# Optimization experiments

Hardware: AMD Instinct MI355X
Metric: run time of the kernel (lower is better)

## Reference

```python
import jax, jax.numpy as jnp
import numpy as np
import math

INPUT_SIZE = 20
HIDDEN = 1500
OUTPUT = 20
MLP_HID = math.ceil(5 / 4 * HIDDEN)  # 1875
T = 4096


def setup_inputs() -> dict:
    key = jax.random.key(0)
    ks = jax.random.split(key, 10)
    s_lstm = 1.0 / np.sqrt(HIDDEN)
    s1 = 1.0 / np.sqrt(HIDDEN)
    s2 = 1.0 / np.sqrt(MLP_HID)
    return {
        "input_seq": jax.random.normal(ks[0], (T, INPUT_SIZE), dtype=jnp.float32),
        "W_ih": jax.random.uniform(ks[1], (4 * HIDDEN, INPUT_SIZE), jnp.float32, -s_lstm, s_lstm),
        "W_hh": jax.random.uniform(ks[2], (4 * HIDDEN, HIDDEN), jnp.float32, -s_lstm, s_lstm),
        "b_ih": jax.random.uniform(ks[3], (4 * HIDDEN,), jnp.float32, -s_lstm, s_lstm),
        "b_hh": jax.random.uniform(ks[4], (4 * HIDDEN,), jnp.float32, -s_lstm, s_lstm),
        "W1": jax.random.uniform(ks[5], (MLP_HID, HIDDEN), jnp.float32, -s1, s1),
        "b1": jax.random.uniform(ks[6], (MLP_HID,), jnp.float32, -s1, s1),
        "W2": jax.random.uniform(ks[7], (OUTPUT, MLP_HID), jnp.float32, -s2, s2),
        "b2": jax.random.uniform(ks[8], (OUTPUT,), jnp.float32, -s2, s2),
    }


def reference(input_seq, W_ih, W_hh, b_ih, b_hh, W1, b1, W2, b2):
    H = W_hh.shape[1]
    # Precompute input contribution for all timesteps: (T, 4H)
    x_proj = input_seq @ W_ih.T + (b_ih + b_hh)

    def step(carry, xp):
        h, c = carry
        gates = xp + h @ W_hh.T  # (4H,)
        i, f, g, o = jnp.split(gates, 4)
        i = jax.nn.sigmoid(i)
        f = jax.nn.sigmoid(f)
        g = jnp.tanh(g)
        o = jax.nn.sigmoid(o)
        c_new = f * c + i * g
        h_new = o * jnp.tanh(c_new)
        return (h_new, c_new), None

    h0 = jnp.zeros((H,), dtype=input_seq.dtype)
    c0 = jnp.zeros((H,), dtype=input_seq.dtype)
    (h_last, _), _ = jax.lax.scan(step, (h0, c0), x_proj)
    # Dropout is identity in eval mode. Module returns predictions[-1],
    # which only depends on the last hidden state.
    hid = h_last @ W1.T + b1
    return hid @ W2.T + b2
```

## Files before the change

kernel.cpp:

```cpp
#include <hip/hip_runtime.h>
#include <math.h>

#define TT 4096
#define HH 1500
#define NB 250
#define NT 512
#define NREP 8

typedef unsigned uv4 __attribute__((ext_vector_type(4)));
typedef _Float16 h2f __attribute__((ext_vector_type(2)));
typedef _Float16 h4f __attribute__((ext_vector_type(4)));

#define ALD4(p)   __hip_atomic_load((p), __ATOMIC_RELAXED, __HIP_MEMORY_SCOPE_AGENT)
#define AST4(p,v) __hip_atomic_store((p), (v), __ATOMIC_RELAXED, __HIP_MEMORY_SCOPE_AGENT)

__device__ __forceinline__ float fast_sigmoid(float z) {
  return 1.0f / (1.0f + __expf(-z));
}
__device__ __forceinline__ float fast_tanh(float z) {
  float az = fabsf(z);
  float e  = __expf(-2.0f * az);
  float r  = (1.0f - e) / (1.0f + e);
  return copysignf(r, z);
}
__device__ __forceinline__ float dot2(unsigned wb, unsigned hb, float acc) {
#if __has_builtin(__builtin_amdgcn_fdot2)
  return __builtin_amdgcn_fdot2(__builtin_bit_cast(h2f, wb),
                                __builtin_bit_cast(h2f, hb), acc, false);
#else
  h2f w = __builtin_bit_cast(h2f, wb), h = __builtin_bit_cast(h2f, hb);
  acc = fmaf((float)w.x, (float)h.x, acc);
  return fmaf((float)w.y, (float)h.y, acc);
#endif
}

__device__ __forceinline__ uv4 pollld(const unsigned* a) {
  uv4 v;
  asm volatile("global_load_dwordx4 %0, %1, off sc0 sc1\n\t"
               "s_waitcnt vmcnt(0)"
               : "=&v"(v) : "v"(a) : "memory");
  return v;
}
__device__ __forceinline__ h4f cvt4h(uv4 v) {
  h4f r;
  r.x = (_Float16)__uint_as_float(v.x);
  r.y = (_Float16)__uint_as_float(v.y);
  r.z = (_Float16)__uint_as_float(v.z);
  r.w = (_Float16)__uint_as_float(v.w);
  return r;
}

__global__
__attribute__((amdgpu_flat_work_group_size(NT, NT), amdgpu_waves_per_eu(2, 2)))
void lstm_fused(
    const float* __restrict__ x,
    const float* __restrict__ Wih,
    const float* __restrict__ Whh,
    const float* __restrict__ bih,
    const float* __restrict__ bhh,
    const float* __restrict__ W1,
    const float* __restrict__ b1,
    const float* __restrict__ W2,
    const float* __restrict__ b2,
    float* __restrict__ out,
    unsigned* __restrict__ ws)
{
  const int tid = threadIdx.x;
  const int bid = blockIdx.x;
  const int wv  = tid >> 6;
  const int ln  = tid & 63;

  unsigned* pub  = ws;
  unsigned* hidp = ws + NREP * 2 * 1536;

  __shared__ __align__(16) _Float16 lds_wh[24 * 1536];
  __shared__ __align__(16) _Float16 lds_hh[1536];
  __shared__ __align__(16) float    lds_hf[1536];
  __shared__ float lds_xp[2][24];
  __shared__ float lds_gs[4][6];
  float* lds_hd = (float*)lds_wh;

  for (int hi = tid; hi < 24 * 1536; hi += NT) {
    const int r = hi / 1536, k = hi - r * 1536;
    const int u = r >> 2, g = r & 3;
    const size_t grow = (size_t)(g * HH + bid * 6 + u) * HH;
    const float v = (k < HH) ? Whh[grow + k] : 0.f;
    lds_wh[hi] = (_Float16)v;
  }
  if (tid < 36) lds_hh[1500 + tid] = (_Float16)0.f;

  const int uu = (wv < 6) ? wv : 0;
  const uv4* wp = ((const uv4*)lds_wh) + (size_t)uu * 4 * 192;
  const uv4* hp = (const uv4*)lds_hh;

  float4 wx0, wx1, wx2, wx3, wx4;
  float4 xr0, xr1, xr2, xr3, xr4;
  float bias = 0.f;
  if (wv == 6 && ln < 24) {
    const int g = ln / 6, u = ln - g * 6;
    const int row = g * HH + bid * 6 + u;
    const float4* s = (const float4*)(Wih + row * 20);
    wx0 = s[0]; wx1 = s[1]; wx2 = s[2]; wx3 = s[3]; wx4 = s[4];
    bias = bih[row] + bhh[row];
    const float4* xx = (const float4*)x;
    xr0 = xx[0]; xr1 = xx[1]; xr2 = xx[2]; xr3 = xx[3]; xr4 = xx[4];
  }

  float c = 0.f;

  if (tid < 6 * NREP)
    AST4(pub + (tid / 6) * 3072 + 6 * bid + (tid % 6), 1u);

  __syncthreads();

  unsigned* myrep = pub + (bid & (NREP - 1)) * 3072;

  for (int t = 0; t < TT; ++t) {
    const int s = t & 1;
    const unsigned tag = (unsigned)((t + 1) & 15);

    uv4 pw[12];
    if (wv < 6) {
      #pragma unroll
      for (int g = 0; g < 4; ++g) {
        #pragma unroll
        for (int m = 0; m < 3; ++m) pw[g * 3 + m] = wp[g * 192 + ln + 64 * m];
      }
      const int ck = (wv << 6) | ln;
      if (ck < 375) {
        unsigned* ap = myrep + s * 1536 + (ck << 2);
        uv4 v;
        for (;;) {
          v = pollld(ap);
          const unsigned miss = ((v.x & 15u) ^ tag) | ((v.y & 15u) ^ tag)
                              | ((v.z & 15u) ^ tag) | ((v.w & 15u) ^ tag);
          if (!miss) break;
          __builtin_amdgcn_s_sleep(1);
        }
        *(h4f*)(lds_hh + (ck << 2)) = cvt4h(v);
      }
    } else if (wv == 6 && ln < 24) {
      float sx = bias;
      sx += wx0.x*xr0.x + wx0.y*xr0.y + wx0.z*xr0.z + wx0.w*xr0.w;
      sx += wx1.x*xr1.x + wx1.y*xr1.y + wx1.z*xr1.z + wx1.w*xr1.w;
      sx += wx2.x*xr2.x + wx2.y*xr2.y + wx2.z*xr2.z + wx2.w*xr2.w;
      sx += wx3.x*xr3.x + wx3.y*xr3.y + wx3.z*xr3.z + wx3.w*xr3.w;
      sx += wx4.x*xr4.x + wx4.y*xr4.y + wx4.z*xr4.z + wx4.w*xr4.w;
      lds_xp[s][ln] = sx;
    }
    __syncthreads();

    if (wv < 6) {
      uv4 hv[3];
      #pragma unroll
      for (int m = 0; m < 3; ++m) hv[m] = hp[ln + 64 * m];
      float a[4] = {0.f, 0.f, 0.f, 0.f};
      #pragma unroll
      for (int g = 0; g < 4; ++g) {
        #pragma unroll
        for (int m = 0; m < 3; ++m) {
          const uv4 q = pw[g * 3 + m], h = hv[m];
          a[g] = dot2(q.x, h.x, a[g]);
          a[g] = dot2(q.y, h.y, a[g]);
          a[g] = dot2(q.z, h.z, a[g]);
          a[g] = dot2(q.w, h.w, a[g]);
        }
      }
      #pragma unroll
      for (int g = 0; g < 4; ++g) {
        a[g] += __shfl_xor(a[g], 16, 64);
        a[g] += __shfl_xor(a[g], 32, 64);
      }
      const int q4 = ln >> 4;
      float v = (q4 == 0) ? a[0] : (q4 == 1) ? a[1] : (q4 == 2) ? a[2] : a[3];
      v += __shfl_xor(v, 1, 64);
      v += __shfl_xor(v, 2, 64);
      v += __shfl_xor(v, 4, 64);
      v += __shfl_xor(v, 8, 64);
      if ((ln & 15) == 0) lds_gs[q4][wv] = v;
    } else if (wv == 6 && ln < 24 && (t + 1) < TT) {
      const float4* xx = (const float4*)(x + 20 * (t + 1));
      xr0 = xx[0]; xr1 = xx[1]; xr2 = xx[2]; xr3 = xx[3]; xr4 = xx[4];
    }
    __syncthreads();

    if (wv == 7) {
      unsigned bits = 0u;
      if (ln < 6) {
        const int u = ln;
        const float zi = lds_gs[0][u] + lds_xp[s][0 + u];
        const float zf = lds_gs[1][u] + lds_xp[s][6 + u];
        const float zg = lds_gs[2][u] + lds_xp[s][12 + u];
        const float zo = lds_gs[3][u] + lds_xp[s][18 + u];
        const float ig = fast_sigmoid(zi);
        const float fg = fast_sigmoid(zf);
        const float gg = fast_tanh(zg);
        const float og = fast_sigmoid(zo);
        c = fg * c + ig * gg;
        const float hn = og * fast_tanh(c);
        bits = (__float_as_uint(hn) & ~15u) | (unsigned)((t + 2) & 15);
      }
      const int u6 = ln % 6;
      const unsigned myb = (unsigned)__shfl((int)bits, u6, 64);
      if (ln < 6 * NREP) {
        const int rep = ln / 6;
        AST4(pub + rep * 3072 + ((t + 1) & 1) * 1536 + 6 * bid + u6, myb);
      }
    }
  }

  {
    const unsigned tagf = (unsigned)((TT + 1) & 15);
    if (tid < 375) {
      unsigned* ap = myrep + (tid << 2);
      uv4 v;
      for (;;) {
        v = pollld(ap);
        const unsigned miss = ((v.x & 15u) ^ tagf) | ((v.y & 15u) ^ tagf)
                            | ((v.z & 15u) ^ tagf) | ((v.w & 15u) ^ tagf);
        if (!miss) break;
        __builtin_amdgcn_s_sleep(1);
      }
      float4 f = {__uint_as_float(v.x), __uint_as_float(v.y),
                  __uint_as_float(v.z), __uint_as_float(v.w)};
      *(float4*)(lds_hf + (tid << 2)) = f;
    } else if (tid < 384) {
      float4 z4 = {0.f, 0.f, 0.f, 0.f};
      *(float4*)(lds_hf + (tid << 2)) = z4;
    }
  }
  __syncthreads();

  {
    const float4* h4 = (const float4*)lds_hf;
    const int r = bid + 250 * wv;
    if (r < 1875) {
      const float4* wrow = (const float4*)(W1 + (size_t)r * HH);
      float ss = 0.f;
      #pragma unroll
      for (int m = 0; m < 6; ++m) {
        const int idx = ln + 64 * m;
        if (idx < 375) {
          const float4 a = wrow[idx], hv = h4[idx];
          ss += a.x*hv.x + a.y*hv.y + a.z*hv.z + a.w*hv.w;
        }
      }
      #pragma unroll
      for (int off = 32; off > 0; off >>= 1) ss += __shfl_xor(ss, off, 64);
      if (ln == 0) {
        const float vv = ss + b1[r];
        AST4(hidp + r, (__float_as_uint(vv) & ~15u) | 5u);
      }
    }
  }
  if (bid != 0) return;

  __syncthreads();
  for (int j = tid; j < 1875; j += NT) {
    unsigned bts;
    for (;;) {
      bts = ALD4(hidp + j);
      if ((bts & 15u) == 5u) break;
      __builtin_amdgcn_s_sleep(1);
    }
    lds_hd[j] = __uint_as_float(bts);
  }
  __syncthreads();

  for (int r = wv; r < 20; r += 8) {
    float ss = 0.f;
    for (int k = ln; k < 1875; k += 64)
      ss = fmaf(W2[(size_t)r * 1875 + k], lds_hd[k], ss);
    #pragma unroll
    for (int off = 32; off > 0; off >>= 1) ss += __shfl_xor(ss, off, 64);
    if (ln == 0) out[r] = ss + b2[r];
  }
}

extern "C" void kernel_launch(void* const* d_in, const int* in_sizes, int n_in,
                              void* d_out, int out_size, void* d_ws, size_t ws_size,
                              hipStream_t stream) {
  const float* x   = (const float*)d_in[0];
  const float* Wih = (const float*)d_in[1];
  const float* Whh = (const float*)d_in[2];
  const float* bih = (const float*)d_in[3];
  const float* bhh = (const float*)d_in[4];
  const float* W1  = (const float*)d_in[5];
  const float* b1  = (const float*)d_in[6];
  const float* W2  = (const float*)d_in[7];
  const float* b2  = (const float*)d_in[8];
  float* out   = (float*)d_out;
  unsigned* ws = (unsigned*)d_ws;

  hipLaunchKernelGGL(lstm_fused, dim3(NB), dim3(NT), 0, stream,
                     x, Wih, Whh, bih, bhh, W1, b1, W2, b2, out, ws);
}
```

Measured before the change: 10.75 ms.

## Pad each block's published hidden slice to its own 64-byte line

The global exchange buffer is re-laid out so each block's six hidden values sit in their own 16-word (64-byte) line instead of being packed contiguously, six per block. The publishing wave now writes that line with 64-bit atomic stores, and each poller reads one line with two 16-byte loads. The aim is to stop several blocks writing into the same cache line, which causes false sharing and extra coherence traffic on the per-step polling path. The cost is a larger buffer, more bytes read per poll, and unaligned 32-bit LDS writes when repacking to fp16. The final readout of the hidden state also drops the zero padding of lds_hf above index 1500, which the later MLP reads may or may not rely on.

```diff
diff --git a/kernel.cpp b/kernel.cpp
--- a/kernel.cpp
+++ b/kernel.cpp
@@ -6,13 +6,15 @@
 #define NB 250
 #define NT 512
 #define NREP 8
+#define LINE 16
+#define SLOT (NB * LINE)
 
 typedef unsigned uv4 __attribute__((ext_vector_type(4)));
 typedef _Float16 h2f __attribute__((ext_vector_type(2)));
-typedef _Float16 h4f __attribute__((ext_vector_type(4)));
 
 #define ALD4(p)   __hip_atomic_load((p), __ATOMIC_RELAXED, __HIP_MEMORY_SCOPE_AGENT)
 #define AST4(p,v) __hip_atomic_store((p), (v), __ATOMIC_RELAXED, __HIP_MEMORY_SCOPE_AGENT)
+#define AST8(p,v) __hip_atomic_store((p), (v), __ATOMIC_RELAXED, __HIP_MEMORY_SCOPE_AGENT)
 
 __device__ __forceinline__ float fast_sigmoid(float z) {
   return 1.0f / (1.0f + __expf(-z));
@@ -34,20 +36,18 @@
 #endif
 }
 
-__device__ __forceinline__ uv4 pollld(const unsigned* a) {
-  uv4 v;
-  asm volatile("global_load_dwordx4 %0, %1, off sc0 sc1\n\t"
+__device__ __forceinline__ void poll2(const unsigned* a0, const unsigned* a1,
+                                      uv4& v0, uv4& v1) {
+  asm volatile("global_load_dwordx4 %0, %2, off sc0 sc1\n\t"
+               "global_load_dwordx4 %1, %3, off sc0 sc1\n\t"
                "s_waitcnt vmcnt(0)"
-               : "=&v"(v) : "v"(a) : "memory");
-  return v;
-}
-__device__ __forceinline__ h4f cvt4h(uv4 v) {
-  h4f r;
-  r.x = (_Float16)__uint_as_float(v.x);
-  r.y = (_Float16)__uint_as_float(v.y);
-  r.z = (_Float16)__uint_as_float(v.z);
-  r.w = (_Float16)__uint_as_float(v.w);
-  return r;
+               : "=&v"(v0), "=&v"(v1) : "v"(a0), "v"(a1) : "memory");
+}
+__device__ __forceinline__ unsigned packh(unsigned a, unsigned b) {
+  h2f p;
+  p.x = (_Float16)__uint_as_float(a);
+  p.y = (_Float16)__uint_as_float(b);
+  return __builtin_bit_cast(unsigned, p);
 }
 
 __global__
@@ -71,7 +71,7 @@
   const int ln  = tid & 63;
 
   unsigned* pub  = ws;
-  unsigned* hidp = ws + NREP * 2 * 1536;
+  unsigned* hidp = ws + NREP * 2 * SLOT;
 
   __shared__ __align__(16) _Float16 lds_wh[24 * 1536];
   __shared__ __align__(16) _Float16 lds_hh[1536];
@@ -108,12 +108,14 @@
 
   float c = 0.f;
 
-  if (tid < 6 * NREP)
-    AST4(pub + (tid / 6) * 3072 + 6 * bid + (tid % 6), 1u);
+  if (tid < 16 * NREP) {
+    const int rep = tid >> 4, k = tid & 15;
+    AST4(pub + rep * (2 * SLOT) + bid * LINE + k, 1u);
+  }
 
   __syncthreads();
 
-  unsigned* myrep = pub + (bid & (NREP - 1)) * 3072;
+  unsigned* myrep = pub + (bid & (NREP - 1)) * (2 * SLOT);
 
   for (int t = 0; t < TT; ++t) {
     const int s = t & 1;
@@ -127,17 +129,21 @@
         for (int m = 0; m < 3; ++m) pw[g * 3 + m] = wp[g * 192 + ln + 64 * m];
       }
       const int ck = (wv << 6) | ln;
-      if (ck < 375) {
-        unsigned* ap = myrep + s * 1536 + (ck << 2);
-        uv4 v;
+      if (ck < NB) {
+        unsigned* ap = myrep + s * SLOT + (ck << 4);
+        uv4 v0, v1;
         for (;;) {
-          v = pollld(ap);
-          const unsigned miss = ((v.x & 15u) ^ tag) | ((v.y & 15u) ^ tag)
-                              | ((v.z & 15u) ^ tag) | ((v.w & 15u) ^ tag);
+          poll2(ap, ap + 4, v0, v1);
+          const unsigned miss = ((v0.x & 15u) ^ tag) | ((v0.y & 15u) ^ tag)
+                              | ((v0.z & 15u) ^ tag) | ((v0.w & 15u) ^ tag)
+                              | ((v1.x & 15u) ^ tag) | ((v1.y & 15u) ^ tag);
           if (!miss) break;
           __builtin_amdgcn_s_sleep(1);
         }
-        *(h4f*)(lds_hh + (ck << 2)) = cvt4h(v);
+        unsigned* hd = (unsigned*)lds_hh;
+        hd[3 * ck]     = packh(v0.x, v0.y);
+        hd[3 * ck + 1] = packh(v0.z, v0.w);
+        hd[3 * ck + 2] = packh(v1.x, v1.y);
       }
     } else if (wv == 6 && ln < 24) {
       float sx = bias;
@@ -200,33 +206,37 @@
         const float hn = og * fast_tanh(c);
         bits = (__float_as_uint(hn) & ~15u) | (unsigned)((t + 2) & 15);
       }
-      const int u6 = ln % 6;
-      const unsigned myb = (unsigned)__shfl((int)bits, u6, 64);
-      if (ln < 6 * NREP) {
-        const int rep = ln / 6;
-        AST4(pub + rep * 3072 + ((t + 1) & 1) * 1536 + 6 * bid + u6, myb);
-      }
+      const unsigned tag2 = (unsigned)((t + 2) & 15);
+      const int rep = ln >> 3, k2 = (ln & 7) << 1;
+      const unsigned s0 = (unsigned)__shfl((int)bits, k2 & 7, 64);
+      const unsigned s1 = (unsigned)__shfl((int)bits, (k2 + 1) & 7, 64);
+      const unsigned d0 = (k2 < 6) ? s0 : tag2;
+      const unsigned d1 = (k2 + 1 < 6) ? s1 : tag2;
+      const unsigned long long dd =
+          (unsigned long long)d0 | ((unsigned long long)d1 << 32);
+      AST8((unsigned long long*)(pub + rep * (2 * SLOT) +
+                                 ((t + 1) & 1) * SLOT + bid * LINE + k2), dd);
     }
   }
 
   {
     const unsigned tagf = (unsigned)((TT + 1) & 15);
-    if (tid < 375) {
-      unsigned* ap = myrep + (tid << 2);
-      uv4 v;
+    if (tid < NB) {
+      unsigned* ap = myrep + (tid << 4);
+      uv4 v0, v1;
       for (;;) {
-        v = pollld(ap);
-        const unsigned miss = ((v.x & 15u) ^ tagf) | ((v.y & 15u) ^ tagf)
-                            | ((v.z & 15u) ^ tagf) | ((v.w & 15u) ^ tagf);
+        poll2(ap, ap + 4, v0, v1);
+        const unsigned miss = ((v0.x & 15u) ^ tagf) | ((v0.y & 15u) ^ tagf)
+                            | ((v0.z & 15u) ^ tagf) | ((v0.w & 15u) ^ tagf)
+                            | ((v1.x & 15u) ^ tagf) | ((v1.y & 15u) ^ tagf);
         if (!miss) break;
         __builtin_amdgcn_s_sleep(1);
       }
-      float4 f = {__uint_as_float(v.x), __uint_as_float(v.y),
-                  __uint_as_float(v.z), __uint_as_float(v.w)};
-      *(float4*)(lds_hf + (tid << 2)) = f;
-    } else if (tid < 384) {
-      float4 z4 = {0.f, 0.f, 0.f, 0.f};
-      *(float4*)(lds_hf + (tid << 2)) = z4;
+      float2* fo = (float2*)(lds_hf + 6 * tid);
+      float2 f0 = {__uint_as_float(v0.x), __uint_as_float(v0.y)};
+      float2 f1 = {__uint_as_float(v0.z), __uint_as_float(v0.w)};
+      float2 f2 = {__uint_as_float(v1.x), __uint_as_float(v1.y)};
+      fo[0] = f0; fo[1] = f1; fo[2] = f2;
     }
   }
   __syncthreads();
```

Result: slower. 11.75 ms (+9.3%).

## Dedicate one wave to h polling, double-buffer h in LDS, fuse gate activation

Applied to the files above, without the earlier changes.

Wave 7 now polls the whole published hidden-state vector with six batched loads per lane and a wave-wide any-check, instead of six compute waves each polling one chunk. The h vector in LDS is double-buffered, and each compute wave applies the gate activations and the cell update itself and publishes its own unit. This removes one __syncthreads per timestep and the lds_gs round trip on the serial critical path. In exchange all polling traffic sits on a single wave and the shuffles per compute wave increase.

```diff
diff --git a/kernel.cpp b/kernel.cpp
--- a/kernel.cpp
+++ b/kernel.cpp
@@ -34,12 +34,26 @@
 #endif
 }
 
-__device__ __forceinline__ uv4 pollld(const unsigned* a) {
-  uv4 v;
-  asm volatile("global_load_dwordx4 %0, %1, off sc0 sc1\n\t"
+__device__ __forceinline__ void poll6(const unsigned* a0, const unsigned* a1,
+                                      const unsigned* a2, const unsigned* a3,
+                                      const unsigned* a4, const unsigned* a5,
+                                      uv4& v0, uv4& v1, uv4& v2,
+                                      uv4& v3, uv4& v4, uv4& v5) {
+  asm volatile("global_load_dwordx4 %0, %6, off sc0 sc1\n\t"
+               "global_load_dwordx4 %1, %7, off sc0 sc1\n\t"
+               "global_load_dwordx4 %2, %8, off sc0 sc1\n\t"
+               "global_load_dwordx4 %3, %9, off sc0 sc1\n\t"
+               "global_load_dwordx4 %4, %10, off sc0 sc1\n\t"
+               "global_load_dwordx4 %5, %11, off sc0 sc1\n\t"
                "s_waitcnt vmcnt(0)"
-               : "=&v"(v) : "v"(a) : "memory");
-  return v;
+               : "=&v"(v0), "=&v"(v1), "=&v"(v2),
+                 "=&v"(v3), "=&v"(v4), "=&v"(v5)
+               : "v"(a0), "v"(a1), "v"(a2), "v"(a3), "v"(a4), "v"(a5)
+               : "memory");
+}
+__device__ __forceinline__ unsigned chk4(uv4 v, unsigned tag) {
+  return ((v.x & 15u) ^ tag) | ((v.y & 15u) ^ tag)
+       | ((v.z & 15u) ^ tag) | ((v.w & 15u) ^ tag);
 }
 __device__ __forceinline__ h4f cvt4h(uv4 v) {
   h4f r;
@@ -74,10 +88,9 @@
   unsigned* hidp = ws + NREP * 2 * 1536;
 
   __shared__ __align__(16) _Float16 lds_wh[24 * 1536];
-  __shared__ __align__(16) _Float16 lds_hh[1536];
+  __shared__ __align__(16) _Float16 lds_hh[2][1536];
   __shared__ __align__(16) float    lds_hf[1536];
   __shared__ float lds_xp[2][24];
-  __shared__ float lds_gs[4][6];
   float* lds_hd = (float*)lds_wh;
 
   for (int hi = tid; hi < 24 * 1536; hi += NT) {
@@ -87,11 +100,10 @@
     const float v = (k < HH) ? Whh[grow + k] : 0.f;
     lds_wh[hi] = (_Float16)v;
   }
-  if (tid < 36) lds_hh[1500 + tid] = (_Float16)0.f;
+  if (tid < 72) lds_hh[tid / 36][1500 + (tid % 36)] = (_Float16)0.f;
 
   const int uu = (wv < 6) ? wv : 0;
   const uv4* wp = ((const uv4*)lds_wh) + (size_t)uu * 4 * 192;
-  const uv4* hp = (const uv4*)lds_hh;
 
   float4 wx0, wx1, wx2, wx3, wx4;
   float4 xr0, xr1, xr2, xr3, xr4;
@@ -99,8 +111,8 @@
   if (wv == 6 && ln < 24) {
     const int g = ln / 6, u = ln - g * 6;
     const int row = g * HH + bid * 6 + u;
-    const float4* s = (const float4*)(Wih + row * 20);
-    wx0 = s[0]; wx1 = s[1]; wx2 = s[2]; wx3 = s[3]; wx4 = s[4];
+    const float4* sp = (const float4*)(Wih + row * 20);
+    wx0 = sp[0]; wx1 = sp[1]; wx2 = sp[2]; wx3 = sp[3]; wx4 = sp[4];
     bias = bih[row] + bhh[row];
     const float4* xx = (const float4*)x;
     xr0 = xx[0]; xr1 = xx[1]; xr2 = xx[2]; xr3 = xx[3]; xr4 = xx[4];
@@ -126,31 +138,45 @@
         #pragma unroll
         for (int m = 0; m < 3; ++m) pw[g * 3 + m] = wp[g * 192 + ln + 64 * m];
       }
-      const int ck = (wv << 6) | ln;
-      if (ck < 375) {
-        unsigned* ap = myrep + s * 1536 + (ck << 2);
-        uv4 v;
-        for (;;) {
-          v = pollld(ap);
-          const unsigned miss = ((v.x & 15u) ^ tag) | ((v.y & 15u) ^ tag)
-                              | ((v.z & 15u) ^ tag) | ((v.w & 15u) ^ tag);
-          if (!miss) break;
-          __builtin_amdgcn_s_sleep(1);
+    } else if (wv == 6) {
+      if (ln < 24) {
+        float sx = bias;
+        sx += wx0.x*xr0.x + wx0.y*xr0.y + wx0.z*xr0.z + wx0.w*xr0.w;
+        sx += wx1.x*xr1.x + wx1.y*xr1.y + wx1.z*xr1.z + wx1.w*xr1.w;
+        sx += wx2.x*xr2.x + wx2.y*xr2.y + wx2.z*xr2.z + wx2.w*xr2.w;
+        sx += wx3.x*xr3.x + wx3.y*xr3.y + wx3.z*xr3.z + wx3.w*xr3.w;
+        sx += wx4.x*xr4.x + wx4.y*xr4.y + wx4.z*xr4.z + wx4.w*xr4.w;
+        lds_xp[s][ln] = sx;
+        if (t + 1 < TT) {
+          const float4* xx = (const float4*)(x + 20 * (t + 1));
+          xr0 = xx[0]; xr1 = xx[1]; xr2 = xx[2]; xr3 = xx[3]; xr4 = xx[4];
         }
-        *(h4f*)(lds_hh + (ck << 2)) = cvt4h(v);
-      }
-    } else if (wv == 6 && ln < 24) {
-      float sx = bias;
-      sx += wx0.x*xr0.x + wx0.y*xr0.y + wx0.z*xr0.z + wx0.w*xr0.w;
-      sx += wx1.x*xr1.x + wx1.y*xr1.y + wx1.z*xr1.z + wx1.w*xr1.w;
-      sx += wx2.x*xr2.x + wx2.y*xr2.y + wx2.z*xr2.z + wx2.w*xr2.w;
-      sx += wx3.x*xr3.x + wx3.y*xr3.y + wx3.z*xr3.z + wx3.w*xr3.w;
-      sx += wx4.x*xr4.x + wx4.y*xr4.y + wx4.z*xr4.z + wx4.w*xr4.w;
-      lds_xp[s][ln] = sx;
+      }
+    } else {
+      const unsigned* bse = myrep + s * 1536 + (ln << 2);
+      const int live5 = (ln < 55);
+      uv4 v0, v1, v2, v3, v4, v5;
+      for (;;) {
+        poll6(bse, bse + 256, bse + 512, bse + 768, bse + 1024, bse + 1280,
+              v0, v1, v2, v3, v4, v5);
+        unsigned miss = chk4(v0, tag) | chk4(v1, tag) | chk4(v2, tag)
+                      | chk4(v3, tag) | chk4(v4, tag);
+        if (live5) miss |= chk4(v5, tag);
+        if (!__any(miss != 0u)) break;
+        __builtin_amdgcn_s_sleep(1);
+      }
+      _Float16* hb = lds_hh[s];
+      *(h4f*)(hb + (ln << 2))        = cvt4h(v0);
+      *(h4f*)(hb + (ln << 2) + 256)  = cvt4h(v1);
+      *(h4f*)(hb + (ln << 2) + 512)  = cvt4h(v2);
+      *(h4f*)(hb + (ln << 2) + 768)  = cvt4h(v3);
+      *(h4f*)(hb + (ln << 2) + 1024) = cvt4h(v4);
+      if (live5) *(h4f*)(hb + (ln << 2) + 1280) = cvt4h(v5);
     }
     __syncthreads();
 
     if (wv < 6) {
+      const uv4* hp = (const uv4*)lds_hh[s];
       uv4 hv[3];
       #pragma unroll
       for (int m = 0; m < 3; ++m) hv[m] = hp[ln + 64 * m];
@@ -177,48 +203,34 @@
       v += __shfl_xor(v, 2, 64);
       v += __shfl_xor(v, 4, 64);
       v += __shfl_xor(v, 8, 64);
-      if ((ln & 15) == 0) lds_gs[q4][wv] = v;
-    } else if (wv == 6 && ln < 24 && (t + 1) < TT) {
-      const float4* xx = (const float4*)(x + 20 * (t + 1));
-      xr0 = xx[0]; xr1 = xx[1]; xr2 = xx[2]; xr3 = xx[3]; xr4 = xx[4];
-    }
-    __syncthreads();
-
-    if (wv == 7) {
+      const float z = v + lds_xp[s][q4 * 6 + wv];
+      const float act = (q4 == 2) ? fast_tanh(z) : fast_sigmoid(z);
+      const float i_ = __shfl(act, 0, 64);
+      const float f_ = __shfl(act, 16, 64);
+      const float g_ = __shfl(act, 32, 64);
+      const float o_ = __shfl(act, 48, 64);
       unsigned bits = 0u;
-      if (ln < 6) {
-        const int u = ln;
-        const float zi = lds_gs[0][u] + lds_xp[s][0 + u];
-        const float zf = lds_gs[1][u] + lds_xp[s][6 + u];
-        const float zg = lds_gs[2][u] + lds_xp[s][12 + u];
-        const float zo = lds_gs[3][u] + lds_xp[s][18 + u];
-        const float ig = fast_sigmoid(zi);
-        const float fg = fast_sigmoid(zf);
-        const float gg = fast_tanh(zg);
-        const float og = fast_sigmoid(zo);
-        c = fg * c + ig * gg;
-        const float hn = og * fast_tanh(c);
+      if (ln == 0) {
+        c = f_ * c + i_ * g_;
+        const float hn = o_ * fast_tanh(c);
         bits = (__float_as_uint(hn) & ~15u) | (unsigned)((t + 2) & 15);
       }
-      const int u6 = ln % 6;
-      const unsigned myb = (unsigned)__shfl((int)bits, u6, 64);
-      if (ln < 6 * NREP) {
-        const int rep = ln / 6;
-        AST4(pub + rep * 3072 + ((t + 1) & 1) * 1536 + 6 * bid + u6, myb);
-      }
+      bits = (unsigned)__shfl((int)bits, 0, 64);
+      if (ln < NREP)
+        AST4(pub + ln * 3072 + ((t + 1) & 1) * 1536 + 6 * bid + wv, bits);
     }
   }
 
   {
     const unsigned tagf = (unsigned)((TT + 1) & 15);
     if (tid < 375) {
-      unsigned* ap = myrep + (tid << 2);
+      const unsigned* ap = myrep + (tid << 2);
       uv4 v;
       for (;;) {
-        v = pollld(ap);
-        const unsigned miss = ((v.x & 15u) ^ tagf) | ((v.y & 15u) ^ tagf)
-                            | ((v.z & 15u) ^ tagf) | ((v.w & 15u) ^ tagf);
-        if (!miss) break;
+        asm volatile("global_load_dwordx4 %0, %1, off sc0 sc1\n\t"
+                     "s_waitcnt vmcnt(0)"
+                     : "=&v"(v) : "v"(ap) : "memory");
+        if (!chk4(v, tagf)) break;
         __builtin_amdgcn_s_sleep(1);
       }
       float4 f = {__uint_as_float(v.x), __uint_as_float(v.y),
```

After: 19.20 ms. +78.6%, slower.
